# Performance work log

Hardware: AMD Instinct MI355X
Metric: run time of the kernel (lower is better)

The kernel has to match this reference:

```python
import jax, jax.numpy as jnp
import numpy as np

B, S, D, H = 2, 2048, 1024, 16
DK = D // H

def setup_inputs() -> dict:
    key = jax.random.key(0)
    ks = jax.random.split(key, 11)
    scale = 1.0 / np.sqrt(D)
    inp = {
        'q': jax.random.normal(ks[0], (B, S, D), jnp.float32),
        'k': jax.random.normal(ks[1], (B, S, D), jnp.float32),
        'v': jax.random.normal(ks[2], (B, S, D), jnp.float32),
        'Wq': jax.random.normal(ks[3], (D, D), jnp.float32) * scale,
        'bq': jnp.zeros((D,), jnp.float32),
        'Wk': jax.random.normal(ks[4], (D, D), jnp.float32) * scale,
        'bk': jnp.zeros((D,), jnp.float32),
        'Wv': jax.random.normal(ks[5], (D, D), jnp.float32) * scale,
        'bv': jnp.zeros((D,), jnp.float32),
        'Wo': jax.random.normal(ks[6], (D, D), jnp.float32) * scale,
        'bo': jnp.zeros((D,), jnp.float32),
    }
    return inp

def reference(q, k, v, Wq, bq, Wk, bk, Wv, bv, Wo, bo):
    # linear projections
    qp = q @ Wq + bq   # [B,S,D]
    kp = k @ Wk + bk
    vp = v @ Wv + bv
    # split heads -> [B,H,S,DK]
    qh = qp.reshape(B, S, H, DK).transpose(0, 2, 1, 3)
    kh = kp.reshape(B, S, H, DK).transpose(0, 2, 1, 3)
    vh = vp.reshape(B, S, H, DK).transpose(0, 2, 1, 3)
    scaled = jnp.einsum('bhqd,bhkd->bhqk', qh, kh) / jnp.sqrt(jnp.float32(DK))
    attn_score = jax.nn.softmax(scaled, axis=-1)  # [B,H,S,S]
    x = jnp.einsum('bhqk,bhkd->bhqd', attn_score, vh)
    # dropout is identity in eval mode
    out = x.transpose(0, 2, 1, 3).reshape(B, S, D)
    return (out @ Wo + bo, attn_score)
```

## Files before the change

kernel.cpp:

```cpp
#include <hip/hip_runtime.h>
#include <hip/hip_bf16.h>
#include <stdint.h>
#include <stddef.h>

typedef unsigned short u16;
typedef __attribute__((ext_vector_type(8))) short short8;
typedef __attribute__((ext_vector_type(4))) short bfx4;
typedef __attribute__((ext_vector_type(4))) float f32x4;
typedef __attribute__((ext_vector_type(4))) float f4;

constexpr int B_ = 2, S_ = 2048, D_ = 1024, H_ = 16;
constexpr size_t OUT_ELEMS = (size_t)B_ * S_ * D_;

__device__ __forceinline__ u16 f2bf(float f) {
    union { float f; unsigned u; } v; v.f = f;
    unsigned r = 0x7FFFu + ((v.u >> 16) & 1u);
    return (u16)((v.u + r) >> 16);
}

__device__ __forceinline__ unsigned cvtpk(float lo, float hi) {
    unsigned r;
    asm("v_cvt_pk_bf16_f32 %0, %1, %2" : "=v"(r) : "v"(lo), "v"(hi));
    return r;
}

__device__ __forceinline__ void gload16(const void* g, void* l) {
    auto gg = reinterpret_cast<const __attribute__((address_space(1))) unsigned*>(
        reinterpret_cast<uintptr_t>(g));
    auto ll = reinterpret_cast<__attribute__((address_space(3))) unsigned*>(
        reinterpret_cast<uintptr_t>(l));
    __builtin_amdgcn_global_load_lds(gg, ll, 16, 0, 0);
}

#define VMWAIT(N) do { asm volatile("s_waitcnt vmcnt(" #N ")" ::: "memory"); } while (0)
__device__ __forceinline__ void barrier_() {
    __builtin_amdgcn_s_barrier();
    __builtin_amdgcn_sched_barrier(0);
}

__global__ __launch_bounds__(256) void cast_kernel(
    const float* __restrict__ q, const float* __restrict__ k, const float* __restrict__ v,
    u16* __restrict__ qo, u16* __restrict__ ko, u16* __restrict__ vo)
{
    const float* src = blockIdx.z == 0 ? q : blockIdx.z == 1 ? k : v;
    u16*         dst = blockIdx.z == 0 ? qo : blockIdx.z == 1 ? ko : vo;
    size_t i = ((size_t)blockIdx.x * 256 + threadIdx.x) * 8;
    f4 a = *(const f4*)(src + i);
    f4 b = *(const f4*)(src + i + 4);
    short8 o;
    o[0]=(short)f2bf(a[0]); o[1]=(short)f2bf(a[1]); o[2]=(short)f2bf(a[2]); o[3]=(short)f2bf(a[3]);
    o[4]=(short)f2bf(b[0]); o[5]=(short)f2bf(b[1]); o[6]=(short)f2bf(b[2]); o[7]=(short)f2bf(b[3]);
    *(short8*)(dst + i) = o;
}

__global__ __launch_bounds__(256) void wtrans_kernel(
    const float* __restrict__ W0, const float* __restrict__ W1,
    const float* __restrict__ W2, const float* __restrict__ W3,
    u16* __restrict__ T0, u16* __restrict__ T1, u16* __restrict__ T2, u16* __restrict__ T3)
{
    __shared__ __align__(16) u16 Ts[64][72];
    const float* W = blockIdx.z == 0 ? W0 : blockIdx.z == 1 ? W1 : blockIdx.z == 2 ? W2 : W3;
    u16*         T = blockIdx.z == 0 ? T0 : blockIdx.z == 1 ? T1 : blockIdx.z == 2 ? T2 : T3;
    const int t = threadIdx.x;
    const int r0 = blockIdx.y * 64, c0 = blockIdx.x * 64;
    const int row = t >> 2, qd = t & 3;

    const float* src = W + (size_t)(r0 + row) * 1024 + c0 + qd * 16;
    u16 tmp[16];
    #pragma unroll
    for (int j = 0; j < 16; j += 4) {
        f4 v = *(const f4*)(src + j);
        tmp[j] = f2bf(v[0]); tmp[j+1] = f2bf(v[1]); tmp[j+2] = f2bf(v[2]); tmp[j+3] = f2bf(v[3]);
    }
    #pragma unroll
    for (int j = 0; j < 16; j++) Ts[row][qd * 16 + j] = tmp[j];
    __syncthreads();
    short8 o0, o1;
    #pragma unroll
    for (int j = 0; j < 8; j++) { o0[j] = (short)Ts[qd*16 + j][row]; o1[j] = (short)Ts[qd*16 + 8 + j][row]; }
    u16* dst = T + (size_t)(c0 + row) * 1024 + r0 + qd * 16;
    *(short8*)dst = o0;
    *(short8*)(dst + 8) = o1;
}

__global__ __launch_bounds__(256) void vtrans_kernel(const u16* __restrict__ vp, u16* __restrict__ vt)
{
    __shared__ __align__(16) u16 Vs[64][72];
    const int t = threadIdx.x;
    const int s0 = blockIdx.x * 64;
    const int bh = blockIdx.y, b = bh >> 4, h = bh & 15;
    #pragma unroll
    for (int i = 0; i < 2; i++) {
        int c = t + 256 * i, row = c >> 3, ch = c & 7;
        *(short8*)(&Vs[row][ch * 8]) =
            *(const short8*)(vp + ((size_t)b * S_ + s0 + row) * D_ + h * 64 + ch * 8);
    }
    __syncthreads();
    #pragma unroll
    for (int i = 0; i < 2; i++) {
        int c = t + 256 * i, d = c >> 3, ch = c & 7;
        short8 o;
        #pragma unroll
        for (int j = 0; j < 8; j++) o[j] = (short)Vs[ch * 8 + j][d];
        *(short8*)(vt + ((size_t)bh * 64 + d) * S_ + s0 + ch * 8) = o;
    }
}

template<int OUT_IS_F32>
__global__ __launch_bounds__(256, 3)
void gemm_bt(const u16* __restrict__ A0, const u16* __restrict__ A1, const u16* __restrict__ A2,
             const u16* __restrict__ Bt0, const u16* __restrict__ Bt1, const u16* __restrict__ Bt2,
             const float* __restrict__ bi0, const float* __restrict__ bi1, const float* __restrict__ bi2,
             void* __restrict__ C0, void* __restrict__ C1, void* __restrict__ C2,
             int M, int N, int K, float sc0, float sc1, float sc2)
{
    __shared__ __align__(16) u16 As[2][128 * 32];
    __shared__ __align__(16) u16 Bs[2][128 * 32];

    const int z = blockIdx.z;
    const u16*   Aptr  = z == 0 ? A0  : z == 1 ? A1  : A2;
    const u16*   Bt    = z == 0 ? Bt0 : z == 1 ? Bt1 : Bt2;
    const float* bias  = z == 0 ? bi0 : z == 1 ? bi1 : bi2;
    void*        Cptr  = z == 0 ? C0  : z == 1 ? C1  : C2;
    const float  scale = z == 0 ? sc0 : z == 1 ? sc1 : sc2;

    const int t = threadIdx.x;
    const int w = t >> 6, l = t & 63, lr = l >> 4, lc = l & 15;
    const int wr = w >> 1, wc = w & 1;
    const int id = blockIdx.y * 8 + blockIdx.x;
    const int xcd = id & 7, i_ = id >> 3;
    const int row0 = ((xcd << 2) | ((i_ >> 4) << 1) | ((i_ >> 3) & 1)) * 128;
    const int col0 = (i_ & 7) * 128;
    const int NI = K >> 5;

    auto issueT = [&](const u16* P, int r0_, int i, u16* dst) {
        #pragma unroll
        for (int j = 0; j < 2; j++) {
            int off = j * 256 + t;
            int row = off >> 2, ch = off & 3;
            const char* src = (const char*)P + (((size_t)(r0_ + row) * K + i * 32) << 1)
                              + ((ch ^ (row & 3)) << 4);
            gload16(src, (char*)dst + off * 16);
        }
    };

    f32x4 acc[4][4] = {};
    issueT(Bt, col0, 0, Bs[0]);
    issueT(Aptr, row0, 0, As[0]);

    for (int i = 0; i < NI; i++) {
        const int p = i & 1;
        if (i + 1 < NI) {
            issueT(Bt, col0, i + 1, Bs[p ^ 1]);
            issueT(Aptr, row0, i + 1, As[p ^ 1]);
            VMWAIT(4);
        } else {
            VMWAIT(0);
        }
        barrier_();

        short8 af[4], bf_[4];
        #pragma unroll
        for (int mm = 0; mm < 4; mm++) {
            int r = wr * 64 + mm * 16 + lc;
            af[mm] = *(const short8*)((const char*)As[p] + r * 64 + ((lr * 16) ^ ((r & 3) << 4)));
        }
        #pragma unroll
        for (int nn = 0; nn < 4; nn++) {
            int r = wc * 64 + nn * 16 + lc;
            bf_[nn] = *(const short8*)((const char*)Bs[p] + r * 64 + ((lr * 16) ^ ((r & 3) << 4)));
        }
        #pragma unroll
        for (int mm = 0; mm < 4; mm++)
            #pragma unroll
            for (int nn = 0; nn < 4; nn++)
                acc[mm][nn] = __builtin_amdgcn_mfma_f32_16x16x32_bf16(af[mm], bf_[nn], acc[mm][nn], 0, 0, 0);
        __builtin_amdgcn_s_barrier();
    }

    float bv[4];
    #pragma unroll
    for (int nn = 0; nn < 4; nn++) bv[nn] = bias[col0 + wc * 64 + nn * 16 + lc];

    #pragma unroll
    for (int mm = 0; mm < 4; mm++) {
        const int row = row0 + wr * 64 + mm * 16 + lr * 4;
        #pragma unroll
        for (int nn = 0; nn < 4; nn++) {
            const int col = col0 + wc * 64 + nn * 16 + lc;
            #pragma unroll
            for (int r = 0; r < 4; r++) {
                float vv = (acc[mm][nn][r] + bv[nn]) * scale;
                if constexpr (OUT_IS_F32) ((float*)Cptr)[(size_t)(row + r) * N + col] = vv;
                else                      ((u16*) Cptr)[(size_t)(row + r) * N + col] = f2bf(vv);
            }
        }
    }
}

__global__ __launch_bounds__(512, 4)
void attn_kernel(const u16* __restrict__ qp, const u16* __restrict__ kp,
                 const u16* __restrict__ vt, float* __restrict__ Pout,
                 u16* __restrict__ xout)
{
    __shared__ __align__(16) u16 Qs[128 * 64];
    __shared__ __align__(16) u16 Ks[2][128 * 64];
    __shared__ __align__(16) u16 Vts[2][64 * 128];

    const int t = threadIdx.x;
    const int w = t >> 6, l = t & 63, lr = l >> 4, lc = l & 15;
    const int bid = blockIdx.x;
    const int s = ((bid & 7) << 6) | (bid >> 3);
    const int q0 = (s & 15) * 128;
    const int bh = s >> 4, b = bh >> 4, h = bh & 15;
    const float L2E = 1.4426950408889634f;
    constexpr int NT = S_ / 128;

    auto issueK = [&](int kt, int buf) {
        #pragma unroll
        for (int i = 0; i < 2; i++) {
            int off = i * 512 + t, row = off >> 3, ch = off & 7;
            const char* src = (const char*)kp + ((((size_t)b * S_ + kt * 128 + row) * D_ + h * 64) << 1)
                              + ((ch ^ (row & 7)) << 4);
            gload16(src, (char*)Ks[buf] + off * 16);
        }
    };
    auto issueV = [&](int kt, int buf) {
        #pragma unroll
        for (int i = 0; i < 2; i++) {
            int off = i * 512 + t, row = off >> 4, ch = off & 15;
            const char* src = (const char*)vt + ((((size_t)bh * 64 + row) * S_ + kt * 128) << 1)
                              + ((ch ^ (row & 7)) << 4);
            gload16(src, (char*)Vts[buf] + off * 16);
        }
    };

    issueK(0, 0);
    #pragma unroll
    for (int i = 0; i < 2; i++) {
        int c = t + 512 * i, row = c >> 3, ch = c & 7;
        short8 vq = *(const short8*)(qp + ((size_t)b * S_ + q0 + row) * D_ + h * 64 + ch * 8);
        *(short8*)((char*)Qs + row * 128 + ((ch * 16) ^ ((row & 7) << 4))) = vq;
    }
    __syncthreads();

    short8 qf[2];
    {
        int r = w * 16 + lc, sw = (r & 7) << 4;
        const char* qb = (const char*)Qs + r * 128;
        qf[0] = *(const short8*)(qb + ((lr * 16) ^ sw));
        qf[1] = *(const short8*)(qb + ((64 + lr * 16) ^ sw));
    }

    float sum = 0.f;
    for (int kt = 0; kt < NT; kt++) {
        const int p = kt & 1;
        if (kt + 1 < NT) { issueK(kt + 1, p ^ 1); VMWAIT(2); }
        else             { VMWAIT(0); }
        barrier_();
        const char* Kb = (const char*)Ks[p];
        #pragma unroll
        for (int f = 0; f < 8; f++) {
            int r = f * 16 + lc, sw = (r & 7) << 4;
            const char* kb = Kb + r * 128;
            short8 k0 = *(const short8*)(kb + ((lr * 16) ^ sw));
            short8 k1 = *(const short8*)(kb + ((64 + lr * 16) ^ sw));
            f32x4 sacc = {};
            sacc = __builtin_amdgcn_mfma_f32_16x16x32_bf16(k0, qf[0], sacc, 0, 0, 0);
            sacc = __builtin_amdgcn_mfma_f32_16x16x32_bf16(k1, qf[1], sacc, 0, 0, 0);
            sum += exp2f(sacc[0] * L2E) + exp2f(sacc[1] * L2E)
                 + exp2f(sacc[2] * L2E) + exp2f(sacc[3] * L2E);
        }
        __builtin_amdgcn_s_barrier();
    }
    issueK(0, 0); issueV(0, 0);
    sum += __shfl_xor(sum, 16);
    sum += __shfl_xor(sum, 32);
    const float inv = 1.0f / sum;

    f32x4 xacc[4] = {};
    float* pbase = Pout + ((size_t)bh * S_ + q0 + w * 16 + lc) * S_ + lr * 4;

    for (int kt = 0; kt < NT; kt++) {
        const int p = kt & 1;
        if (kt + 1 < NT) { issueK(kt + 1, p ^ 1); issueV(kt + 1, p ^ 1); }
        if (kt == 0)           VMWAIT(4);
        else if (kt + 1 < NT)  VMWAIT(12);
        else                   VMWAIT(8);
        barrier_();
        const char* Kb = (const char*)Ks[p];
        const char* Vb = (const char*)Vts[p];

        #pragma unroll
        for (int kk = 0; kk < 4; kk++) {
            union { unsigned u[4]; short8 s8; } pu;
            #pragma unroll
            for (int fo = 0; fo < 2; fo++) {
                const int f = kk * 2 + fo;
                int r = f * 16 + lc, sw = (r & 7) << 4;
                const char* kb = Kb + r * 128;
                short8 k0 = *(const short8*)(kb + ((lr * 16) ^ sw));
                short8 k1 = *(const short8*)(kb + ((64 + lr * 16) ^ sw));
                f32x4 sacc = {};
                __builtin_amdgcn_s_setprio(1);
                sacc = __builtin_amdgcn_mfma_f32_16x16x32_bf16(k0, qf[0], sacc, 0, 0, 0);
                sacc = __builtin_amdgcn_mfma_f32_16x16x32_bf16(k1, qf[1], sacc, 0, 0, 0);
                __builtin_amdgcn_s_setprio(0);
                f32x4 pv_;
                pv_[0] = exp2f(sacc[0] * L2E) * inv;
                pv_[1] = exp2f(sacc[1] * L2E) * inv;
                pv_[2] = exp2f(sacc[2] * L2E) * inv;
                pv_[3] = exp2f(sacc[3] * L2E) * inv;
                *(f32x4*)(pbase + (size_t)kt * 128 + f * 16) = pv_;
                pu.u[fo * 2 + 0] = cvtpk(pv_[0], pv_[1]);
                pu.u[fo * 2 + 1] = cvtpk(pv_[2], pv_[3]);
            }
            const short8 pa = pu.s8;
            __builtin_amdgcn_s_setprio(1);
            #pragma unroll
            for (int n = 0; n < 4; n++) {
                int rr = n * 16 + lc, sw2 = (rr & 7) << 4;
                const char* vrow = Vb + rr * 256;
                union { bfx4 h[2]; short8 s8; } vu;
                vu.h[0] = *(const bfx4*)(vrow + ((kk * 64 + lr * 8) ^ sw2));
                vu.h[1] = *(const bfx4*)(vrow + ((kk * 64 + 32 + lr * 8) ^ sw2));
                xacc[n] = __builtin_amdgcn_mfma_f32_16x16x32_bf16(pa, vu.s8, xacc[n], 0, 0, 0);
            }
            __builtin_amdgcn_s_setprio(0);
        }
        __builtin_amdgcn_s_barrier();
    }

    #pragma unroll
    for (int n = 0; n < 4; n++) {
        #pragma unroll
        for (int r = 0; r < 4; r++) {
            int row = q0 + w * 16 + lr * 4 + r;
            int col = h * 64 + n * 16 + lc;
            xout[((size_t)b * S_ + row) * D_ + col] = f2bf(xacc[n][r]);
        }
    }
}

extern "C" void kernel_launch(void* const* d_in, const int* in_sizes, int n_in,
                              void* d_out, int out_size, void* d_ws, size_t ws_size,
                              hipStream_t stream)
{
    const float* qin = (const float*)d_in[0];
    const float* kin = (const float*)d_in[1];
    const float* vin = (const float*)d_in[2];
    const float* Wq  = (const float*)d_in[3];
    const float* bq  = (const float*)d_in[4];
    const float* Wk  = (const float*)d_in[5];
    const float* bk  = (const float*)d_in[6];
    const float* Wv  = (const float*)d_in[7];
    const float* bv  = (const float*)d_in[8];
    const float* Wo  = (const float*)d_in[9];
    const float* bo  = (const float*)d_in[10];

    u16* base = (u16*)d_ws;
    u16* Wqt = base;
    u16* Wkt = base + 1048576;
    u16* Wvt = base + 2097152;
    u16* Wot = base + 3145728;
    u16* qpb = base + 4194304;
    u16* kpb = base + 8388608;
    u16* vpb = base + 12582912;
    u16* vtb = base + 16777216;
    u16* xb  = base + 20971520;
    u16* qcb = base + 25165824;
    u16* kcb = base + 29360128;
    u16* vcb = base + 33554432;

    float* out  = (float*)d_out;
    float* Pout = out + OUT_ELEMS;

    const int M = B_ * S_;

    wtrans_kernel<<<dim3(16, 16, 4), 256, 0, stream>>>(Wq, Wk, Wv, Wo, Wqt, Wkt, Wvt, Wot);
    cast_kernel<<<dim3(2048, 1, 3), 256, 0, stream>>>(qin, kin, vin, qcb, kcb, vcb);
    gemm_bt<0><<<dim3(8, 32, 3), 256, 0, stream>>>(
        qcb, kcb, vcb, Wqt, Wkt, Wvt, bq, bk, bv, qpb, kpb, vpb, M, D_, D_, 0.125f, 1.0f, 1.0f);
    vtrans_kernel<<<dim3(32, 32), 256, 0, stream>>>(vpb, vtb);
    attn_kernel<<<512, 512, 0, stream>>>(qpb, kpb, vtb, Pout, xb);
    gemm_bt<1><<<dim3(8, 32, 1), 256, 0, stream>>>(
        xb, xb, xb, Wot, Wot, Wot, bo, bo, bo, out, out, out, M, D_, D_, 1.0f, 1.0f, 1.0f);
}
```

Before: 273.9 us.

## Fuse input bf16 cast and V transpose into QKV projection GEMM

Removes the standalone fp32-to-bf16 cast kernel and the V transpose kernel. The QKV GEMM now loads fp32 activations through registers, converts them, and stores them into swizzled LDS. The V projection epilogue writes its output directly in transposed [b,h,d,s] layout. This saves two launches and the round trips through intermediate buffers. In exchange, the A operand is staged through registers instead of async global-to-LDS loads, which may reduce load/compute overlap, and the transposed V stores are less coalesced.

Result: slower. 281.1 us (+2.6%).

```diff
diff --git a/kernel.cpp b/kernel.cpp
--- a/kernel.cpp
+++ b/kernel.cpp
@@ -36,21 +36,6 @@
 __device__ __forceinline__ void barrier_() {
     __builtin_amdgcn_s_barrier();
     __builtin_amdgcn_sched_barrier(0);
-}
-
-__global__ __launch_bounds__(256) void cast_kernel(
-    const float* __restrict__ q, const float* __restrict__ k, const float* __restrict__ v,
-    u16* __restrict__ qo, u16* __restrict__ ko, u16* __restrict__ vo)
-{
-    const float* src = blockIdx.z == 0 ? q : blockIdx.z == 1 ? k : v;
-    u16*         dst = blockIdx.z == 0 ? qo : blockIdx.z == 1 ? ko : vo;
-    size_t i = ((size_t)blockIdx.x * 256 + threadIdx.x) * 8;
-    f4 a = *(const f4*)(src + i);
-    f4 b = *(const f4*)(src + i + 4);
-    short8 o;
-    o[0]=(short)f2bf(a[0]); o[1]=(short)f2bf(a[1]); o[2]=(short)f2bf(a[2]); o[3]=(short)f2bf(a[3]);
-    o[4]=(short)f2bf(b[0]); o[5]=(short)f2bf(b[1]); o[6]=(short)f2bf(b[2]); o[7]=(short)f2bf(b[3]);
-    *(short8*)(dst + i) = o;
 }
 
 __global__ __launch_bounds__(256) void wtrans_kernel(
@@ -83,46 +68,45 @@
     *(short8*)(dst + 8) = o1;
 }
 
-__global__ __launch_bounds__(256) void vtrans_kernel(const u16* __restrict__ vp, u16* __restrict__ vt)
+struct Stage { short8 h[2]; };
+
+__device__ __forceinline__ void stage_load_f32(Stage& st, const float* Af, int row0, int K, int k0, int t) {
+    const int row = t >> 1, half = t & 1;
+    const float* p = Af + (size_t)(row0 + row) * K + k0 + half * 16;
+    #pragma unroll
+    for (int j = 0; j < 2; j++) {
+        f4 v0 = *(const f4*)(p + j * 8);
+        f4 v1 = *(const f4*)(p + j * 8 + 4);
+        short8 hh;
+        hh[0]=(short)f2bf(v0[0]); hh[1]=(short)f2bf(v0[1]); hh[2]=(short)f2bf(v0[2]); hh[3]=(short)f2bf(v0[3]);
+        hh[4]=(short)f2bf(v1[0]); hh[5]=(short)f2bf(v1[1]); hh[6]=(short)f2bf(v1[2]); hh[7]=(short)f2bf(v1[3]);
+        st.h[j] = hh;
+    }
+}
+
+__device__ __forceinline__ void stage_store_f32(const Stage& st, u16* Ls, int t) {
+    const int row = t >> 1, half = t & 1;
+    #pragma unroll
+    for (int j = 0; j < 2; j++) {
+        int byteo = half * 32 + j * 16;
+        *(short8*)((char*)Ls + row * 64 + (byteo ^ ((row & 3) << 4))) = st.h[j];
+    }
+}
+
+__global__ __launch_bounds__(256, 3)
+void gemm_qkv(const float* __restrict__ A0, const float* __restrict__ A1, const float* __restrict__ A2,
+              const u16* __restrict__ Bt0, const u16* __restrict__ Bt1, const u16* __restrict__ Bt2,
+              const float* __restrict__ bi0, const float* __restrict__ bi1, const float* __restrict__ bi2,
+              u16* __restrict__ Cq, u16* __restrict__ Ck, u16* __restrict__ Vt)
 {
-    __shared__ __align__(16) u16 Vs[64][72];
-    const int t = threadIdx.x;
-    const int s0 = blockIdx.x * 64;
-    const int bh = blockIdx.y, b = bh >> 4, h = bh & 15;
-    #pragma unroll
-    for (int i = 0; i < 2; i++) {
-        int c = t + 256 * i, row = c >> 3, ch = c & 7;
-        *(short8*)(&Vs[row][ch * 8]) =
-            *(const short8*)(vp + ((size_t)b * S_ + s0 + row) * D_ + h * 64 + ch * 8);
-    }
-    __syncthreads();
-    #pragma unroll
-    for (int i = 0; i < 2; i++) {
-        int c = t + 256 * i, d = c >> 3, ch = c & 7;
-        short8 o;
-        #pragma unroll
-        for (int j = 0; j < 8; j++) o[j] = (short)Vs[ch * 8 + j][d];
-        *(short8*)(vt + ((size_t)bh * 64 + d) * S_ + s0 + ch * 8) = o;
-    }
-}
-
-template<int OUT_IS_F32>
-__global__ __launch_bounds__(256, 3)
-void gemm_bt(const u16* __restrict__ A0, const u16* __restrict__ A1, const u16* __restrict__ A2,
-             const u16* __restrict__ Bt0, const u16* __restrict__ Bt1, const u16* __restrict__ Bt2,
-             const float* __restrict__ bi0, const float* __restrict__ bi1, const float* __restrict__ bi2,
-             void* __restrict__ C0, void* __restrict__ C1, void* __restrict__ C2,
-             int M, int N, int K, float sc0, float sc1, float sc2)
-{
+    constexpr int K = D_, N = D_;
     __shared__ __align__(16) u16 As[2][128 * 32];
     __shared__ __align__(16) u16 Bs[2][128 * 32];
 
     const int z = blockIdx.z;
-    const u16*   Aptr  = z == 0 ? A0  : z == 1 ? A1  : A2;
-    const u16*   Bt    = z == 0 ? Bt0 : z == 1 ? Bt1 : Bt2;
-    const float* bias  = z == 0 ? bi0 : z == 1 ? bi1 : bi2;
-    void*        Cptr  = z == 0 ? C0  : z == 1 ? C1  : C2;
-    const float  scale = z == 0 ? sc0 : z == 1 ? sc1 : sc2;
+    const float* Aptr = z == 0 ? A0  : z == 1 ? A1  : A2;
+    const u16*   Bt   = z == 0 ? Bt0 : z == 1 ? Bt1 : Bt2;
+    const float* bias = z == 0 ? bi0 : z == 1 ? bi1 : bi2;
 
     const int t = threadIdx.x;
     const int w = t >> 6, l = t & 63, lr = l >> 4, lc = l & 15;
@@ -133,6 +117,103 @@
     const int col0 = (i_ & 7) * 128;
     const int NI = K >> 5;
 
+    auto issueB = [&](int i, u16* dst) {
+        #pragma unroll
+        for (int j = 0; j < 2; j++) {
+            int off = j * 256 + t;
+            int row = off >> 2, ch = off & 3;
+            const char* src = (const char*)Bt + (((size_t)(col0 + row) * K + i * 32) << 1)
+                              + ((ch ^ (row & 3)) << 4);
+            gload16(src, (char*)dst + off * 16);
+        }
+    };
+
+    f32x4 acc[4][4] = {};
+    Stage sa;
+    issueB(0, Bs[0]);
+    stage_load_f32(sa, Aptr, row0, K, 0, t);
+
+    for (int i = 0; i < NI; i++) {
+        const int p = i & 1;
+        stage_store_f32(sa, As[p], t);
+        __syncthreads();
+        if (i + 1 < NI) {
+            issueB(i + 1, Bs[p ^ 1]);
+            stage_load_f32(sa, Aptr, row0, K, (i + 1) * 32, t);
+        }
+
+        short8 af[4], bf_[4];
+        #pragma unroll
+        for (int mm = 0; mm < 4; mm++) {
+            int r = wr * 64 + mm * 16 + lc;
+            af[mm] = *(const short8*)((const char*)As[p] + r * 64 + ((lr * 16) ^ ((r & 3) << 4)));
+        }
+        #pragma unroll
+        for (int nn = 0; nn < 4; nn++) {
+            int r = wc * 64 + nn * 16 + lc;
+            bf_[nn] = *(const short8*)((const char*)Bs[p] + r * 64 + ((lr * 16) ^ ((r & 3) << 4)));
+        }
+        #pragma unroll
+        for (int mm = 0; mm < 4; mm++)
+            #pragma unroll
+            for (int nn = 0; nn < 4; nn++)
+                acc[mm][nn] = __builtin_amdgcn_mfma_f32_16x16x32_bf16(af[mm], bf_[nn], acc[mm][nn], 0, 0, 0);
+        __builtin_amdgcn_s_barrier();
+    }
+
+    float bv[4];
+    #pragma unroll
+    for (int nn = 0; nn < 4; nn++) bv[nn] = bias[col0 + wc * 64 + nn * 16 + lc];
+
+    if (z == 2) {
+        #pragma unroll
+        for (int mm = 0; mm < 4; mm++) {
+            const int row = row0 + wr * 64 + mm * 16 + lr * 4;
+            const int b = row >> 11, s = row & 2047;
+            #pragma unroll
+            for (int nn = 0; nn < 4; nn++) {
+                const int col = col0 + wc * 64 + nn * 16 + lc;
+                const int h = col >> 6, d = col & 63;
+                bfx4 o;
+                #pragma unroll
+                for (int r = 0; r < 4; r++) o[r] = (short)f2bf(acc[mm][nn][r] + bv[nn]);
+                *(bfx4*)(Vt + (((size_t)((b * 16 + h) * 64 + d)) << 11) + s) = o;
+            }
+        }
+    } else {
+        u16* Cptr = z == 0 ? Cq : Ck;
+        const float scale = z == 0 ? 0.125f : 1.0f;
+        #pragma unroll
+        for (int mm = 0; mm < 4; mm++) {
+            const int row = row0 + wr * 64 + mm * 16 + lr * 4;
+            #pragma unroll
+            for (int nn = 0; nn < 4; nn++) {
+                const int col = col0 + wc * 64 + nn * 16 + lc;
+                #pragma unroll
+                for (int r = 0; r < 4; r++)
+                    Cptr[(size_t)(row + r) * N + col] = f2bf((acc[mm][nn][r] + bv[nn]) * scale);
+            }
+        }
+    }
+}
+
+__global__ __launch_bounds__(256, 3)
+void gemm_out(const u16* __restrict__ Aptr, const u16* __restrict__ Bt,
+              const float* __restrict__ bias, float* __restrict__ Cptr)
+{
+    constexpr int K = D_, N = D_;
+    __shared__ __align__(16) u16 As[2][128 * 32];
+    __shared__ __align__(16) u16 Bs[2][128 * 32];
+
+    const int t = threadIdx.x;
+    const int w = t >> 6, l = t & 63, lr = l >> 4, lc = l & 15;
+    const int wr = w >> 1, wc = w & 1;
+    const int id = blockIdx.y * 8 + blockIdx.x;
+    const int xcd = id & 7, i_ = id >> 3;
+    const int row0 = ((xcd << 2) | ((i_ >> 4) << 1) | ((i_ >> 3) & 1)) * 128;
+    const int col0 = (i_ & 7) * 128;
+    const int NI = K >> 5;
+
     auto issueT = [&](const u16* P, int r0_, int i, u16* dst) {
         #pragma unroll
         for (int j = 0; j < 2; j++) {
@@ -189,11 +270,8 @@
         for (int nn = 0; nn < 4; nn++) {
             const int col = col0 + wc * 64 + nn * 16 + lc;
             #pragma unroll
-            for (int r = 0; r < 4; r++) {
-                float vv = (acc[mm][nn][r] + bv[nn]) * scale;
-                if constexpr (OUT_IS_F32) ((float*)Cptr)[(size_t)(row + r) * N + col] = vv;
-                else                      ((u16*) Cptr)[(size_t)(row + r) * N + col] = f2bf(vv);
-            }
+            for (int r = 0; r < 4; r++)
+                Cptr[(size_t)(row + r) * N + col] = acc[mm][nn][r] + bv[nn];
         }
     }
 }
@@ -365,24 +443,15 @@
     u16* Wot = base + 3145728;
     u16* qpb = base + 4194304;
     u16* kpb = base + 8388608;
-    u16* vpb = base + 12582912;
-    u16* vtb = base + 16777216;
-    u16* xb  = base + 20971520;
-    u16* qcb = base + 25165824;
-    u16* kcb = base + 29360128;
-    u16* vcb = base + 33554432;
+    u16* vtb = base + 12582912;
+    u16* xb  = base + 16777216;
 
     float* out  = (float*)d_out;
     float* Pout = out + OUT_ELEMS;
 
-    const int M = B_ * S_;
-
     wtrans_kernel<<<dim3(16, 16, 4), 256, 0, stream>>>(Wq, Wk, Wv, Wo, Wqt, Wkt, Wvt, Wot);
-    cast_kernel<<<dim3(2048, 1, 3), 256, 0, stream>>>(qin, kin, vin, qcb, kcb, vcb);
-    gemm_bt<0><<<dim3(8, 32, 3), 256, 0, stream>>>(
-        qcb, kcb, vcb, Wqt, Wkt, Wvt, bq, bk, bv, qpb, kpb, vpb, M, D_, D_, 0.125f, 1.0f, 1.0f);
-    vtrans_kernel<<<dim3(32, 32), 256, 0, stream>>>(vpb, vtb);
+    gemm_qkv<<<dim3(8, 32, 3), 256, 0, stream>>>(
+        qin, kin, vin, Wqt, Wkt, Wvt, bq, bk, bv, qpb, kpb, vtb);
     attn_kernel<<<512, 512, 0, stream>>>(qpb, kpb, vtb, Pout, xb);
-    gemm_bt<1><<<dim3(8, 32, 1), 256, 0, stream>>>(
-        xb, xb, xb, Wot, Wot, Wot, bo, bo, bo, out, out, out, M, D_, D_, 1.0f, 1.0f, 1.0f);
-}
+    gemm_out<<<dim3(8, 32), 256, 0, stream>>>(xb, Wot, bo, out);
+}
```
